# Kernel optimization log

Hardware: AMD Instinct MI355X
Metric: run time of the kernel (lower is better)

Reference implementation:

```python
import jax, jax.numpy as jnp
import numpy as np

NUM_HEADS = 4

def _ln(h, g, b, eps=1e-5):
    m = jnp.mean(h, axis=-1, keepdims=True)
    v = jnp.var(h, axis=-1, keepdims=True)
    return (h - m) / jnp.sqrt(v + eps) * g + b

def setup_inputs() -> dict:
    N, E, dn, de, da, H = 10000, 320000, 128, 128, 128, NUM_HEADS
    d_n, d_e, d_o = dn // H, de // H, da // H
    keys = iter(jax.random.split(jax.random.key(0), 64))
    def rn(shape, s=0.02):
        return jax.random.normal(next(keys), shape, dtype=jnp.float32) * s
    inp = {
        'x': jax.random.normal(next(keys), (N, dn), dtype=jnp.float32),
        'edge_feature': jax.random.normal(next(keys), (E, de), dtype=jnp.float32),
        'edge_index': jax.random.randint(next(keys), (2, E), 0, N, dtype=jnp.int32),
        # edge_gate: Linear(de, de//2) -> ReLU -> BN(eval, identity stats) -> Linear(de//2, 1) -> Sigmoid
        'Wg1': rn((de, de // 2)), 'bg1': jnp.zeros((de // 2,), jnp.float32),
        'Wg2': rn((de // 2, 1)), 'bg2': jnp.zeros((1,), jnp.float32),
        # nn_edge: build_mlp([2dn+2de, dn+2de, de]), Linear-ReLU-Linear
        'We1': rn((2 * dn + 2 * de, dn + 2 * de)), 'be1': jnp.zeros((dn + 2 * de,), jnp.float32),
        'We2': rn((dn + 2 * de, de)), 'be2': jnp.zeros((de,), jnp.float32),
        # edge LayerNorm
        'ge': jnp.ones((de,), jnp.float32), 'beta_e': jnp.zeros((de,), jnp.float32),
        # projections (single Linear each)
        'Wq': rn((dn, dn)), 'bq': jnp.zeros((dn,), jnp.float32),
        'Wpe': rn((de, de)), 'bpe': jnp.zeros((de,), jnp.float32),
        'Wv': rn((dn, da)), 'bv': jnp.zeros((da,), jnp.float32),
        # attention MLP (Conv1d kernel-1 over channel dim): [d_n+d_e, d_n+d_e, d_o]
        'A1': rn((d_n + d_e, d_n + d_e)), 'a1': jnp.zeros((d_n + d_e,), jnp.float32),
        'A2': rn((d_o, d_n + d_e)), 'a2': jnp.zeros((d_o,), jnp.float32),
        # twinning linear (shared; original re-inits per node, see notes): [2*de -> da]
        'Wt': rn((2 * de, da)), 'bt': jnp.zeros((da,), jnp.float32),
        # prop: build_mlp([dn+da, dn+da, dn])
        'Wp1': rn((dn + da, dn + da)), 'bp1': jnp.zeros((dn + da,), jnp.float32),
        'Wp2': rn((dn + da, dn)), 'bp2': jnp.zeros((dn,), jnp.float32),
        # final LayerNorm
        'gn': jnp.ones((dn,), jnp.float32), 'bn': jnp.zeros((dn,), jnp.float32),
    }
    return inp

def reference(x, edge_feature, edge_index, Wg1, bg1, Wg2, bg2, We1, be1, We2, be2,
              ge, beta_e, Wq, bq, Wpe, bpe, Wv, bv, A1, a1, A2, a2, Wt, bt,
              Wp1, bp1, Wp2, bp2, gn, bn):
    N, E = x.shape[0], edge_index.shape[1]
    H = NUM_HEADS
    src, dst = edge_index[0], edge_index[1]
    x_i = x[src]            # [E, dn]  (flow target_to_source: i = edge_index[0])
    x_j = x[dst]            # [E, dn]
    # --- reverse-edge lookup, vectorized via sorted key search ---
    key = src.astype(jnp.int64) * N + dst.astype(jnp.int64)
    rkey = dst.astype(jnp.int64) * N + src.astype(jnp.int64)
    order = jnp.argsort(key)
    sk = key[order]
    pos = jnp.clip(jnp.searchsorted(sk, rkey), 0, E - 1)
    found = sk[pos] == rkey
    rev_feat = jnp.where(found[:, None], edge_feature[order[pos]], 0.0)
    # --- edge gate (BatchNorm in eval with default stats == identity) ---
    g = jax.nn.relu(edge_feature @ Wg1 + bg1)
    gates = jax.nn.sigmoid(g @ Wg2 + bg2)   # [E,1]
    rev_feat = gates * rev_feat
    # --- MultiHeadedEdgeAttention ---
    ef = jnp.concatenate([x_i, edge_feature, rev_feat, x_j], axis=1)  # [E, 2dn+2de]
    ef = jax.nn.relu(ef @ We1 + be1) @ We2 + be2
    gcn_edge_feature = _ln(ef, ge, beta_e)                            # [E, de]
    value = x_j @ Wv + bv                                             # [E, da]
    q = (x_i @ Wq + bq).reshape(E, -1, H)                             # [E, d_n, H]
    e = (edge_feature @ Wpe + bpe).reshape(E, -1, H)                  # [E, d_e, H]
    h = jnp.concatenate([q, e], axis=1)                               # [E, d_n+d_e, H]
    h = jax.nn.relu(jnp.einsum('bch,oc->boh', h, A1) + a1[None, :, None])
    prob = jnp.einsum('bch,oc->boh', h, A2) + a2[None, :, None]       # [E, d_o, H]
    prob = jax.nn.softmax(prob, axis=1)
    xx_e = prob.reshape(E, -1) * value                                # [E, da]
    # --- scatter-max aggregate at src (dim_size N), empty segments -> 0 ---
    seg = jax.ops.segment_max(xx_e, src, num_segments=N)
    ones = jnp.ones((E,), jnp.float32)
    cnt_s = jax.ops.segment_sum(ones, src, num_segments=N)
    cnt_d = jax.ops.segment_sum(ones, dst, num_segments=N)
    xx = jnp.where(cnt_s[:, None] > 0, seg, 0.0)                      # [N, da]
    # --- twinning edge attention: mean of gcn edge features per subject/object ---
    subj = jax.ops.segment_sum(gcn_edge_feature, src, num_segments=N) / jnp.maximum(cnt_s, 1.0)[:, None]
    obj = jax.ops.segment_sum(gcn_edge_feature, dst, num_segments=N) / jnp.maximum(cnt_d, 1.0)[:, None]
    twin = jnp.concatenate([subj, obj], axis=1) @ Wt + bt             # [N, da]
    xx = jax.nn.relu(xx) * jax.nn.sigmoid(twin)
    xx = jnp.concatenate([x, xx], axis=1)
    xx = jax.nn.relu(xx @ Wp1 + bp1) @ Wp2 + bp2
    xx = _ln(xx, gn, bn)
    return (xx, gcn_edge_feature)
```

## Files before the change

### kernel.cpp

```cpp
#include <hip/hip_runtime.h>

#define N_NODES 10000
#define N_EDGES 320000
#define HASH_LOG 20
#define HASH_SZ (1 << HASH_LOG)
#define HASH_MASK (HASH_SZ - 1)
#define EMPTY_KEY 0xFFFFFFFFu

typedef unsigned int u32;
typedef unsigned short u16;
typedef __attribute__((ext_vector_type(8))) short bf16x8;
typedef __attribute__((ext_vector_type(4))) float f32x4;

__device__ __forceinline__ float bf2f(u16 v) {
    return __uint_as_float(((u32)v) << 16);
}
__device__ __forceinline__ u16 f2b(float f) {
    u32 x = __float_as_uint(f);
    return (u16)((x + 0x7FFFu + ((x >> 16) & 1u)) >> 16);
}
__device__ __forceinline__ void unpack8(uint4 u, float* f) {
    f[0] = __uint_as_float(u.x << 16); f[1] = __uint_as_float(u.x & 0xFFFF0000u);
    f[2] = __uint_as_float(u.y << 16); f[3] = __uint_as_float(u.y & 0xFFFF0000u);
    f[4] = __uint_as_float(u.z << 16); f[5] = __uint_as_float(u.z & 0xFFFF0000u);
    f[6] = __uint_as_float(u.w << 16); f[7] = __uint_as_float(u.w & 0xFFFF0000u);
}
__device__ __forceinline__ bf16x8 pack8(float4 a, float4 b) {
    union { bf16x8 v; u32 u[4]; } r;
    r.u[0] = (u32)f2b(a.x) | ((u32)f2b(a.y) << 16);
    r.u[1] = (u32)f2b(a.z) | ((u32)f2b(a.w) << 16);
    r.u[2] = (u32)f2b(b.x) | ((u32)f2b(b.y) << 16);
    r.u[3] = (u32)f2b(b.z) | ((u32)f2b(b.w) << 16);
    return r.v;
}

__global__ __launch_bounds__(256) void k_hash_build(
    const int* __restrict__ ei, u32* __restrict__ hkey, int* __restrict__ hval,
    int* __restrict__ cs, int* __restrict__ cd)
{
    int e = blockIdx.x * 256 + threadIdx.x;
    int s = ei[e], d = ei[N_EDGES + e];
    atomicAdd(&cs[s], 1);
    atomicAdd(&cd[d], 1);
    u32 key = (u32)(s * N_NODES + d);
    u32 h = (key * 2654435761u) >> (32 - HASH_LOG);
    for (;;) {
        u32 prev = atomicCAS(&hkey[h], EMPTY_KEY, key);
        if (prev == EMPTY_KEY || prev == key) { atomicMin(&hval[h], e); break; }
        h = (h + 1) & HASH_MASK;
    }
}

__global__ __launch_bounds__(256) void k_rev_lookup(
    const int* __restrict__ ei, const u32* __restrict__ hkey,
    const int* __restrict__ hval, int* __restrict__ rev)
{
    int e = blockIdx.x * 256 + threadIdx.x;
    int s = ei[e], d = ei[N_EDGES + e];
    u32 rkey = (u32)(d * N_NODES + s);
    u32 h = (rkey * 2654435761u) >> (32 - HASH_LOG);
    int r = -1;
    for (;;) {
        u32 k = hkey[h];
        if (k == EMPTY_KEY) break;
        if (k == rkey) { r = hval[h]; break; }
        h = (h + 1) & HASH_MASK;
    }
    rev[e] = r;
}

__global__ __launch_bounds__(256) void k_scan(
    const int* __restrict__ cs, const int* __restrict__ cd,
    int* __restrict__ off_s, int* __restrict__ off_d)
{
    __shared__ int sums[256];
    const int t = threadIdx.x;
    const int C = 40;
    const int* src = (blockIdx.x == 0) ? cs : cd;
    int* dst = (blockIdx.x == 0) ? off_s : off_d;
    int lo = t * C;
    int s = 0;
    for (int i = 0; i < C; i++) {
        int idx = lo + i;
        if (idx < N_NODES) s += src[idx];
    }
    sums[t] = s;
    __syncthreads();
    if (t == 0) {
        int acc = 0;
        for (int i = 0; i < 256; i++) { int v = sums[i]; sums[i] = acc; acc += v; }
    }
    __syncthreads();
    int acc = sums[t];
    for (int i = 0; i < C; i++) {
        int idx = lo + i;
        if (idx < N_NODES) { dst[idx] = acc; acc += src[idx]; }
    }
    if (t == 0) dst[N_NODES] = N_EDGES;
}

__global__ __launch_bounds__(256) void k_bucket(
    const int* __restrict__ ei, const int* __restrict__ off_s,
    const int* __restrict__ off_d, int* __restrict__ cur_s,
    int* __restrict__ cur_d, int* __restrict__ csr_es, int* __restrict__ csr_ed)
{
    int e = blockIdx.x * 256 + threadIdx.x;
    int s = ei[e], d = ei[N_EDGES + e];
    int ps = off_s[s] + atomicAdd(&cur_s[s], 1);
    csr_es[ps] = e;
    int pd = off_d[d] + atomicAdd(&cur_d[d], 1);
    csr_ed[pd] = e;
}

__global__ __launch_bounds__(256) void k_wconv(
    const float* __restrict__ src, u16* __restrict__ dst, int n)
{
    int i = blockIdx.x * 256 + threadIdx.x;
    if (i < n) dst[i] = f2b(src[i]);
}

__global__ __launch_bounds__(256) void k_wpackfrag(
    const float* __restrict__ src, u16* __restrict__ dst,
    int K, int Nn, int r0, int ld)
{
    int g = blockIdx.x * 256 + threadIdx.x;
    int ntc = Nn >> 4;
    int total = (K >> 5) * ntc * 64;
    if (g >= total) return;
    int lane = g & 63;
    int f = g >> 6;
    int nt = f % ntc, kc = f / ntc;
    int lq = lane & 15, q8 = lane >> 4;
    const float* s = src + (size_t)(r0 + kc * 32 + q8 * 8) * ld + nt * 16 + lq;
    u32 out[4];
#pragma unroll
    for (int j = 0; j < 4; j++) {
        float v0 = s[(size_t)(2 * j) * ld], v1 = s[(size_t)(2 * j + 1) * ld];
        out[j] = (u32)f2b(v0) | ((u32)f2b(v1) << 16);
    }
    *(uint4*)(dst + (size_t)g * 8) = make_uint4(out[0], out[1], out[2], out[3]);
}

__global__ __launch_bounds__(256) void k_node_proj(
    const float* __restrict__ x,
    const float* __restrict__ Wq, const float* __restrict__ bq,
    const float* __restrict__ Wv, const float* __restrict__ bv,
    const float* __restrict__ We1, const float* __restrict__ be1,
    u16* __restrict__ xq, u16* __restrict__ xv,
    u16* __restrict__ Pn, u16* __restrict__ Qn)
{
    __shared__ float XT[128 * 36];
    __shared__ float Ws[16 * 128];
    const int t = threadIdx.x;
    const int nb = blockIdx.x, y = blockIdx.y;
    const int n0 = nb * 32;
    {
        int nl = t & 31;
        int n = n0 + nl; if (n >= N_NODES) n = N_NODES - 1;
        int k0 = (t >> 5) * 16;
        const float4* xp = (const float4*)(x + (size_t)n * 128 + k0);
#pragma unroll
        for (int i = 0; i < 4; i++) {
            float4 v = xp[i];
            XT[(k0 + 4 * i + 0) * 36 + nl] = v.x;
            XT[(k0 + 4 * i + 1) * 36 + nl] = v.y;
            XT[(k0 + 4 * i + 2) * 36 + nl] = v.z;
            XT[(k0 + 4 * i + 3) * 36 + nl] = v.w;
        }
    }
    const int col = t & 127, rb = t >> 7;
    float acc[16];
#pragma unroll
    for (int j = 0; j < 16; j++) acc[j] = 0.f;
    for (int kc = 0; kc < 8; kc++) {
        __syncthreads();
#pragma unroll
        for (int i = 0; i < 2; i++) {
            int f4 = t + 256 * i;
            int row = f4 >> 5, c4 = (f4 & 31) * 4;
            int kg = kc * 16 + row;
            const float* srcw;
            if (y == 0)      srcw = Wq + (size_t)kg * 128 + c4;
            else if (y == 1) srcw = Wv + (size_t)kg * 128 + c4;
            else if (y < 5)  srcw = We1 + (size_t)kg * 384 + (y - 2) * 128 + c4;
            else             srcw = We1 + (size_t)(384 + kg) * 384 + (y - 5) * 128 + c4;
            *(float4*)&Ws[row * 128 + c4] = *(const float4*)srcw;
        }
        __syncthreads();
#pragma unroll
        for (int k = 0; k < 16; k++) {
            float w = Ws[k * 128 + col];
            const float4* ap = (const float4*)&XT[(kc * 16 + k) * 36 + rb * 16];
            float4 a0 = ap[0], a1v = ap[1], a2v = ap[2], a3v = ap[3];
            float ar[16] = {a0.x,a0.y,a0.z,a0.w, a1v.x,a1v.y,a1v.z,a1v.w,
                            a2v.x,a2v.y,a2v.z,a2v.w, a3v.x,a3v.y,a3v.z,a3v.w};
#pragma unroll
            for (int j = 0; j < 16; j++) acc[j] = fmaf(ar[j], w, acc[j]);
        }
    }
    float bias = 0.f;
    if (y == 0) bias = bq[col];
    else if (y == 1) bias = bv[col];
    else if (y < 5) bias = be1[(y - 2) * 128 + col];
#pragma unroll
    for (int j = 0; j < 16; j++) {
        int n = n0 + rb * 16 + j;
        if (n >= N_NODES) continue;
        u16 v = f2b(acc[j] + bias);
        if (y == 0)      xq[(size_t)n * 128 + col] = v;
        else if (y == 1) xv[(size_t)n * 128 + col] = v;
        else if (y < 5)  Pn[(size_t)n * 384 + (y - 2) * 128 + col] = v;
        else             Qn[(size_t)n * 384 + (y - 5) * 128 + col] = v;
    }
}

__global__ __launch_bounds__(256) void k_gates(
    const float* __restrict__ ef,
    const float* __restrict__ Wg1, const float* __restrict__ bg1,
    const float* __restrict__ Wg2, const float* __restrict__ bg2,
    float* __restrict__ gates)
{
    __shared__ float Wg1s[128 * 64];
    __shared__ float EFT[32 * 68];
    const int t = threadIdx.x;
    const int e0 = blockIdx.x * 64;
#pragma unroll
    for (int i = 0; i < 8; i++) {
        int f4 = t + 256 * i;
        *(float4*)&Wg1s[f4 * 4] = *(const float4*)&Wg1[f4 * 4];
    }
    const int o = t & 63, eb = t >> 6;
    float acc[16];
#pragma unroll
    for (int j = 0; j < 16; j++) acc[j] = 0.f;
    for (int kc = 0; kc < 4; kc++) {
        __syncthreads();
        {
            int e = t & 63, kk = (t >> 6) * 8;
            const float4* p = (const float4*)&ef[(size_t)(e0 + e) * 128 + kc * 32 + kk];
            float4 v0 = p[0], v1 = p[1];
            EFT[(kk + 0) * 68 + e] = v0.x; EFT[(kk + 1) * 68 + e] = v0.y;
            EFT[(kk + 2) * 68 + e] = v0.z; EFT[(kk + 3) * 68 + e] = v0.w;
            EFT[(kk + 4) * 68 + e] = v1.x; EFT[(kk + 5) * 68 + e] = v1.y;
            EFT[(kk + 6) * 68 + e] = v1.z; EFT[(kk + 7) * 68 + e] = v1.w;
        }
        __syncthreads();
#pragma unroll
        for (int k = 0; k < 32; k++) {
            const float4* ap = (const float4*)&EFT[k * 68 + eb * 16];
            float4 a0 = ap[0], a1v = ap[1], a2v = ap[2], a3v = ap[3];
            float w = Wg1s[(kc * 32 + k) * 64 + o];
            float ar[16] = {a0.x,a0.y,a0.z,a0.w, a1v.x,a1v.y,a1v.z,a1v.w,
                            a2v.x,a2v.y,a2v.z,a2v.w, a3v.x,a3v.y,a3v.z,a3v.w};
#pragma unroll
            for (int j = 0; j < 16; j++) acc[j] = fmaf(ar[j], w, acc[j]);
        }
    }
    float b1 = bg1[o], w2 = Wg2[o], b2 = bg2[0];
#pragma unroll
    for (int j = 0; j < 16; j++) {
        float v = fmaxf(acc[j] + b1, 0.f) * w2;
#pragma unroll
        for (int off = 32; off > 0; off >>= 1) v += __shfl_xor(v, off, 64);
        if ((t & 63) == 0)
            gates[e0 + eb * 16 + j] = 1.f / (1.f + __expf(-(v + b2)));
    }
}

__global__ __launch_bounds__(256, 3) void k_edge_mlp(
    const float* __restrict__ ef, const int* __restrict__ ei,
    const int* __restrict__ rev, const float* __restrict__ gates,
    const u16* __restrict__ Pn, const u16* __restrict__ Qn,
    const u16* __restrict__ We1p, const u16* __restrict__ We2p,
    const float* __restrict__ be2, const float* __restrict__ ge,
    const float* __restrict__ beta_e,
    float* __restrict__ out_gcn)
{
    __shared__ char ldsbuf[50176];
    __shared__ int srcs[64], dsts[64], revs[64];
    __shared__ float gts[64];
    u16* Abuf = (u16*)ldsbuf;
    u16* H1   = (u16*)ldsbuf;

    const int t = threadIdx.x;
    const int e0 = blockIdx.x * 64;
    const int w = t >> 6, lane = t & 63, q8 = lane >> 4, lq = lane & 15;

    if (t < 64) {
        srcs[t] = ei[e0 + t]; dsts[t] = ei[N_EDGES + e0 + t];
        revs[t] = rev[e0 + t]; gts[t] = gates[e0 + t];
    }
    __syncthreads();
    {
        int r = t >> 2, part = t & 3;
        int e = e0 + r;
        u16* arow = Abuf + r * 264;
        const float* efr = ef + (size_t)e * 128 + part * 32;
#pragma unroll
        for (int i = 0; i < 8; i++) {
            float4 v = *(const float4*)(efr + i * 4);
            u32 lo = (u32)f2b(v.x) | ((u32)f2b(v.y) << 16);
            u32 hi = (u32)f2b(v.z) | ((u32)f2b(v.w) << 16);
            *(uint2*)&arow[part * 32 + i * 4] = make_uint2(lo, hi);
        }
        int rv = revs[r];
        float g = gts[r];
        if (rv >= 0) {
            const float* rr = ef + (size_t)rv * 128 + part * 32;
#pragma unroll
            for (int i = 0; i < 8; i++) {
                float4 v = *(const float4*)(rr + i * 4);
                u32 lo = (u32)f2b(v.x * g) | ((u32)f2b(v.y * g) << 16);
                u32 hi = (u32)f2b(v.z * g) | ((u32)f2b(v.w * g) << 16);
                *(uint2*)&arow[128 + part * 32 + i * 4] = make_uint2(lo, hi);
            }
        } else {
#pragma unroll
            for (int i = 0; i < 8; i++)
                *(uint2*)&arow[128 + part * 32 + i * 4] = make_uint2(0u, 0u);
        }
    }
    __syncthreads();
    f32x4 acc1[4][6];
#pragma unroll
    for (int mt = 0; mt < 4; mt++)
#pragma unroll
        for (int nt = 0; nt < 6; nt++) acc1[mt][nt] = (f32x4){0.f, 0.f, 0.f, 0.f};
    {
        const u16* Bp = We1p + ((size_t)(w * 6) * 64 + lane) * 8;
#pragma unroll 2
        for (int kc = 0; kc < 8; kc++) {
            bf16x8 af[4], bfr[6];
#pragma unroll
            for (int mt = 0; mt < 4; mt++)
                af[mt] = *(const bf16x8*)(Abuf + (mt * 16 + lq) * 264 + kc * 32 + q8 * 8);
#pragma unroll
            for (int nt = 0; nt < 6; nt++)
                bfr[nt] = *(const bf16x8*)(Bp + (size_t)kc * 12288 + nt * 512);
#pragma unroll
            for (int mt = 0; mt < 4; mt++)
#pragma unroll
                for (int nt = 0; nt < 6; nt++)
                    acc1[mt][nt] = __builtin_amdgcn_mfma_f32_16x16x32_bf16(
                        af[mt], bfr[nt], acc1[mt][nt], 0, 0, 0);
        }
    }
    __syncthreads();
#pragma unroll
    for (int mt = 0; mt < 4; mt++) {
        int m = mt * 16 + q8 * 4;
#pragma unroll
        for (int nt = 0; nt < 6; nt++) {
            int c = w * 96 + nt * 16 + lq;
#pragma unroll
            for (int r = 0; r < 4; r++)
                H1[(m + r) * 392 + c] = f2b(acc1[mt][nt][r]);
        }
    }
    __syncthreads();
    {
        int r = t >> 2, cb = (t & 3) * 96;
        const u16* pr = Pn + (size_t)srcs[r] * 384;
        const u16* qr = Qn + (size_t)dsts[r] * 384;
        u16* hr = H1 + r * 392;
#pragma unroll
        for (int i = 0; i < 12; i++) {
            int c = cb + i * 8;
            uint4 hv = *(uint4*)&hr[c];
            uint4 pv = *(const uint4*)&pr[c];
            uint4 qv = *(const uint4*)&qr[c];
            float hf[8], pf[8], qf[8];
            unpack8(hv, hf); unpack8(pv, pf); unpack8(qv, qf);
            u16 o[8];
#pragma unroll
            for (int j = 0; j < 8; j++) o[j] = f2b(fmaxf(hf[j] + pf[j] + qf[j], 0.f));
            uint4 ov;
            ov.x = (u32)o[0] | ((u32)o[1] << 16);
            ov.y = (u32)o[2] | ((u32)o[3] << 16);
            ov.z = (u32)o[4] | ((u32)o[5] << 16);
            ov.w = (u32)o[6] | ((u32)o[7] << 16);
            *(uint4*)&hr[c] = ov;
        }
    }
    __syncthreads();
    f32x4 acc2[8];
#pragma unroll
    for (int nt = 0; nt < 8; nt++) acc2[nt] = (f32x4){0.f, 0.f, 0.f, 0.f};
    {
        const u16* Bp2 = We2p + (size_t)lane * 8;
#pragma unroll 2
        for (int kc = 0; kc < 12; kc++) {
            bf16x8 a = *(const bf16x8*)(H1 + (w * 16 + lq) * 392 + kc * 32 + q8 * 8);
#pragma unroll
            for (int nt = 0; nt < 8; nt++) {
                bf16x8 b = *(const bf16x8*)(Bp2 + (size_t)kc * 4096 + nt * 512);
                acc2[nt] = __builtin_amdgcn_mfma_f32_16x16x32_bf16(a, b, acc2[nt], 0, 0, 0);
            }
        }
    }
    {
        float be2v[8], gev[8], bev[8];
#pragma unroll
        for (int nt = 0; nt < 8; nt++) {
            int c = nt * 16 + lq;
            be2v[nt] = be2[c]; gev[nt] = ge[c]; bev[nt] = beta_e[c];
        }
#pragma unroll
        for (int r = 0; r < 4; r++) {
            int m = w * 16 + q8 * 4 + r;
            int e = e0 + m;
            float vals[8];
            float s = 0.f, sq = 0.f;
#pragma unroll
            for (int nt = 0; nt < 8; nt++) {
                float v = acc2[nt][r] + be2v[nt];
                vals[nt] = v; s += v; sq += v * v;
            }
#pragma unroll
            for (int off = 8; off > 0; off >>= 1) {
                s += __shfl_xor(s, off, 64);
                sq += __shfl_xor(sq, off, 64);
            }
            float mean = s * (1.f / 128.f);
            float var = sq * (1.f / 128.f) - mean * mean;
            float rstd = rsqrtf(var + 1e-5f);
            float* og = out_gcn + (size_t)e * 128;
#pragma unroll
            for (int nt = 0; nt < 8; nt++) {
                int c = nt * 16 + lq;
                og[c] = (vals[nt] - mean) * rstd * gev[nt] + bev[nt];
            }
        }
    }
}

__device__ __forceinline__ int hswz(int r, int c) {
    int g = ((c >> 3) ^ r ^ (r >> 3)) & 7;
    return r * 128 + (g << 4) + ((c & 7) << 1);
}

__global__ __launch_bounds__(256, 5) void k_atten(
    const float* __restrict__ ef, const int* __restrict__ ei,
    const u16* __restrict__ xq, const u16* __restrict__ xv,
    const u16* __restrict__ Wpep, const float* __restrict__ bpe,
    const u16* __restrict__ A1b, const float* __restrict__ a1,
    const u16* __restrict__ A2b, const float* __restrict__ a2,
    u16* __restrict__ xxe)
{
    __shared__ __align__(16) char lds[32768];
    const int t = threadIdx.x;
    const int e0 = blockIdx.x * 64;
    const int w = t >> 6, lane = t & 63, q8 = lane >> 4, lq = lane & 15;
    char* Hw = lds + w * 8192;
    const int ew0 = e0 + w * 16;

    {
        int el = lane >> 2, part = lane & 3;
        int sn = ei[ew0 + el];
        const uint4* p = (const uint4*)(xq + (size_t)sn * 128 + part * 32);
        int r0 = el * 4;
#pragma unroll
        for (int i = 0; i < 4; i++) {
            uint4 v = p[i];
            int c0 = part * 8 + i * 2;
            *(u32*)(Hw + hswz(r0 + 0, c0)) = (v.x & 0xFFFFu) | (v.z << 16);
            *(u32*)(Hw + hswz(r0 + 1, c0)) = (v.x >> 16) | (v.z & 0xFFFF0000u);
            *(u32*)(Hw + hswz(r0 + 2, c0)) = (v.y & 0xFFFFu) | (v.w << 16);
            *(u32*)(Hw + hswz(r0 + 3, c0)) = (v.y >> 16) | (v.w & 0xFFFF0000u);
        }
    }
    f32x4 acc1[8];
#pragma unroll
    for (int nt = 0; nt < 8; nt++) acc1[nt] = (f32x4){0.f, 0.f, 0.f, 0.f};
    {
        const u16* Bp = Wpep + (size_t)lane * 8;
#pragma unroll
        for (int kc = 0; kc < 4; kc++) {
            const float* ar = ef + (size_t)(ew0 + lq) * 128 + kc * 32 + q8 * 8;
            float4 v0 = ((const float4*)ar)[0];
            float4 v1 = ((const float4*)ar)[1];
            bf16x8 a = pack8(v0, v1);
#pragma unroll
            for (int nt = 0; nt < 8; nt++) {
                bf16x8 b = *(const bf16x8*)(Bp + (size_t)(kc * 8 + nt) * 512);
                acc1[nt] = __builtin_amdgcn_mfma_f32_16x16x32_bf16(
                    a, b, acc1[nt], 0, 0, 0);
            }
        }
    }
    {
#pragma unroll
        for (int nt = 0; nt < 8; nt++) {
            int j = nt * 16 + lq;
            int c = 32 + (j >> 2), hh = j & 3;
            float bb = bpe[j];
#pragma unroll
            for (int r = 0; r < 4; r++) {
                int el = q8 * 4 + r;
                *(u16*)(Hw + hswz(el * 4 + hh, c)) = f2b(acc1[nt][r] + bb);
            }
        }
    }
    f32x4 acc2[4][4];
#pragma unroll
    for (int mt = 0; mt < 4; mt++)
#pragma unroll
        for (int nt = 0; nt < 4; nt++) acc2[mt][nt] = (f32x4){0.f, 0.f, 0.f, 0.f};
#pragma unroll
    for (int kc = 0; kc < 2; kc++) {
        bf16x8 af[4], bfr[4];
#pragma unroll
        for (int mt = 0; mt < 4; mt++)
            af[mt] = *(const bf16x8*)(Hw + hswz(mt * 16 + lq, kc * 32 + q8 * 8));
#pragma unroll
        for (int nt = 0; nt < 4; nt++)
            bfr[nt] = *(const bf16x8*)(A1b + (size_t)(nt * 16 + lq) * 64 + kc * 32 + q8 * 8);
#pragma unroll
        for (int mt = 0; mt < 4; mt++)
#pragma unroll
            for (int nt = 0; nt < 4; nt++)
                acc2[mt][nt] = __builtin_amdgcn_mfma_f32_16x16x32_bf16(
                    af[mt], bfr[nt], acc2[mt][nt], 0, 0, 0);
    }
    {
        float a1v[4];
#pragma unroll
        for (int nt = 0; nt < 4; nt++) a1v[nt] = a1[nt * 16 + lq];
#pragma unroll
        for (int mt = 0; mt < 4; mt++)
#pragma unroll
            for (int nt = 0; nt < 4; nt++)
#pragma unroll
                for (int r = 0; r < 4; r++)
                    *(u16*)(Hw + hswz(mt * 16 + q8 * 4 + r, nt * 16 + lq)) =
                        f2b(fmaxf(acc2[mt][nt][r] + a1v[nt], 0.f));
    }
    f32x4 acc3[4][2];
#pragma unroll
    for (int mt = 0; mt < 4; mt++)
#pragma unroll
        for (int nt = 0; nt < 2; nt++) acc3[mt][nt] = (f32x4){0.f, 0.f, 0.f, 0.f};
#pragma unroll
    for (int kc = 0; kc < 2; kc++) {
        bf16x8 af[4], bfr[2];
#pragma unroll
        for (int mt = 0; mt < 4; mt++)
            af[mt] = *(const bf16x8*)(Hw + hswz(mt * 16 + lq, kc * 32 + q8 * 8));
#pragma unroll
        for (int nt = 0; nt < 2; nt++)
            bfr[nt] = *(const bf16x8*)(A2b + (size_t)(nt * 16 + lq) * 64 + kc * 32 + q8 * 8);
#pragma unroll
        for (int mt = 0; mt < 4; mt++)
#pragma unroll
            for (int nt = 0; nt < 2; nt++)
                acc3[mt][nt] = __builtin_amdgcn_mfma_f32_16x16x32_bf16(
                    af[mt], bfr[nt], acc3[mt][nt], 0, 0, 0);
    }
    {
        float a2v0 = a2[lq], a2v1 = a2[16 + lq];
#pragma unroll
        for (int mt = 0; mt < 4; mt++) {
#pragma unroll
            for (int r = 0; r < 4; r++) {
                float v0 = acc3[mt][0][r] + a2v0;
                float v1 = acc3[mt][1][r] + a2v1;
                float m = fmaxf(v0, v1);
#pragma unroll
                for (int off = 1; off < 16; off <<= 1)
                    m = fmaxf(m, __shfl_xor(m, off, 16));
                float p0 = __expf(v0 - m), p1 = __expf(v1 - m);
                float s = p0 + p1;
#pragma unroll
                for (int off = 1; off < 16; off <<= 1)
                    s += __shfl_xor(s, off, 16);
                float inv = 1.f / s;
                acc3[mt][0][r] = p0 * inv;
                acc3[mt][1][r] = p1 * inv;
            }
        }
    }
#pragma unroll
    for (int mt = 0; mt < 4; mt++) {
        int e = ew0 + mt * 4 + q8;
        int dn = ei[N_EDGES + e];
        const u16* vr = xv + (size_t)dn * 128;
        u16* xe = xxe + (size_t)e * 128;
#pragma unroll
        for (int nt = 0; nt < 2; nt++) {
            int o = nt * 16 + lq;
            uint2 vv = *(const uint2*)(vr + o * 4);
            float vf[4];
            vf[0] = bf2f((u16)(vv.x & 0xFFFFu)); vf[1] = bf2f((u16)(vv.x >> 16));
            vf[2] = bf2f((u16)(vv.y & 0xFFFFu)); vf[3] = bf2f((u16)(vv.y >> 16));
            u16 ov[4];
#pragma unroll
            for (int r = 0; r < 4; r++)
                ov[r] = f2b(fmaxf(acc3[mt][nt][r] * vf[r], 0.f));
            uint2 pk;
            pk.x = (u32)ov[0] | ((u32)ov[1] << 16);
            pk.y = (u32)ov[2] | ((u32)ov[3] << 16);
            *(uint2*)(xe + o * 4) = pk;
        }
    }
}

__global__ __launch_bounds__(256) void k_aggregate(
    const int* __restrict__ off_s, const int* __restrict__ off_d,
    const int* __restrict__ csr_es, const int* __restrict__ csr_ed,
    const u16* __restrict__ xxe, const float* __restrict__ gcn,
    float* __restrict__ xx, float* __restrict__ subj, float* __restrict__ obj)
{
    const int t = threadIdx.x;
    const int lane = t & 63, w = t >> 6;
    const int n = blockIdx.x * 4 + w;
    int s0 = off_s[n], s1 = off_s[n + 1];
    float mx0 = 0.f, mx1 = 0.f;
    float sb0 = 0.f, sb1 = 0.f;
    for (int i = s0; i < s1; i++) {
        int e = csr_es[i];
        u32 v = *(const u32*)(xxe + (size_t)e * 128 + 2 * lane);
        mx0 = fmaxf(mx0, bf2f((u16)(v & 0xFFFFu)));
        mx1 = fmaxf(mx1, bf2f((u16)(v >> 16)));
        float2 g = *(const float2*)&gcn[(size_t)e * 128 + 2 * lane];
        sb0 += g.x; sb1 += g.y;
    }
    int d0 = off_d[n], d1 = off_d[n + 1];
    float ob0 = 0.f, ob1 = 0.f;
    for (int i = d0; i < d1; i++) {
        int e = csr_ed[i];
        float2 g = *(const float2*)&gcn[(size_t)e * 128 + 2 * lane];
        ob0 += g.x; ob1 += g.y;
    }
    *(float2*)&xx[(size_t)n * 128 + 2 * lane] = make_float2(mx0, mx1);
    *(float2*)&subj[(size_t)n * 128 + 2 * lane] = make_float2(sb0, sb1);
    *(float2*)&obj[(size_t)n * 128 + 2 * lane] = make_float2(ob0, ob1);
}

__global__ __launch_bounds__(256) void k_node_final(
    const float* __restrict__ x, const float* __restrict__ subj,
    const float* __restrict__ obj, const int* __restrict__ cs,
    const int* __restrict__ cd, const float* __restrict__ xxbuf,
    const float* __restrict__ Wt, const float* __restrict__ bt,
    const float* __restrict__ Wp1, const float* __restrict__ bp1,
    const float* __restrict__ Wp2, const float* __restrict__ bp2,
    const float* __restrict__ gn, const float* __restrict__ bn,
    float* __restrict__ out)
{
    __shared__ float sc[4][4][256];
    const int t = threadIdx.x;
    const int lane = t & 63, w = t >> 6;
    const int n0 = blockIdx.x * 16 + w * 4;
#pragma unroll
    for (int nn = 0; nn < 4; nn++) {
        int n = n0 + nn;
        float inv_s = 1.f / fmaxf((float)cs[n], 1.f);
        float inv_d = 1.f / fmaxf((float)cd[n], 1.f);
#pragma unroll
        for (int i = 0; i < 4; i++) {
            int c = lane + 64 * i;
            float v = (c < 128) ? subj[(size_t)n * 128 + c] * inv_s
                                : obj[(size_t)n * 128 + (c - 128)] * inv_d;
            sc[w][nn][c] = v;
        }
    }
    __syncthreads();
    float a8[4][2];
#pragma unroll
    for (int nn = 0; nn < 4; nn++) { a8[nn][0] = 0.f; a8[nn][1] = 0.f; }
#pragma unroll 4
    for (int k = 0; k < 256; k++) {
        float2 wv = *(const float2*)&Wt[(size_t)k * 128 + 2 * lane];
#pragma unroll
        for (int nn = 0; nn < 4; nn++) {
            float h = sc[w][nn][k];
            a8[nn][0] = fmaf(h, wv.x, a8[nn][0]);
            a8[nn][1] = fmaf(h, wv.y, a8[nn][1]);
        }
    }
    __syncthreads();
    {
        float bt0 = bt[2 * lane], bt1 = bt[2 * lane + 1];
#pragma unroll
        for (int nn = 0; nn < 4; nn++) {
            int n = n0 + nn;
            float tw0 = a8[nn][0] + bt0, tw1 = a8[nn][1] + bt1;
            float xx0 = xxbuf[(size_t)n * 128 + 2 * lane] * (1.f / (1.f + __expf(-tw0)));
            float xx1 = xxbuf[(size_t)n * 128 + 2 * lane + 1] * (1.f / (1.f + __expf(-tw1)));
            float2 xv2 = *(const float2*)&x[(size_t)n * 128 + 2 * lane];
            sc[w][nn][2 * lane] = xv2.x;
            sc[w][nn][2 * lane + 1] = xv2.y;
            sc[w][nn][128 + 2 * lane] = xx0;
            sc[w][nn][129 + 2 * lane] = xx1;
        }
    }
    __syncthreads();
    float a16[4][4];
#pragma unroll
    for (int nn = 0; nn < 4; nn++)
#pragma unroll
        for (int j = 0; j < 4; j++) a16[nn][j] = 0.f;
#pragma unroll 4
    for (int k = 0; k < 256; k++) {
        float4 wv = *(const float4*)&Wp1[(size_t)k * 256 + 4 * lane];
#pragma unroll
        for (int nn = 0; nn < 4; nn++) {
            float h = sc[w][nn][k];
            a16[nn][0] = fmaf(h, wv.x, a16[nn][0]);
            a16[nn][1] = fmaf(h, wv.y, a16[nn][1]);
            a16[nn][2] = fmaf(h, wv.z, a16[nn][2]);
            a16[nn][3] = fmaf(h, wv.w, a16[nn][3]);
        }
    }
    __syncthreads();
    {
        float q0 = bp1[4 * lane], q1 = bp1[4 * lane + 1];
        float q2 = bp1[4 * lane + 2], q3 = bp1[4 * lane + 3];
#pragma unroll
        for (int nn = 0; nn < 4; nn++) {
            sc[w][nn][4 * lane + 0] = fmaxf(a16[nn][0] + q0, 0.f);
            sc[w][nn][4 * lane + 1] = fmaxf(a16[nn][1] + q1, 0.f);
            sc[w][nn][4 * lane + 2] = fmaxf(a16[nn][2] + q2, 0.f);
            sc[w][nn][4 * lane + 3] = fmaxf(a16[nn][3] + q3, 0.f);
        }
    }
    __syncthreads();
    float a8b[4][2];
#pragma unroll
    for (int nn = 0; nn < 4; nn++) { a8b[nn][0] = 0.f; a8b[nn][1] = 0.f; }
#pragma unroll 4
    for (int k = 0; k < 256; k++) {
        float2 wv = *(const float2*)&Wp2[(size_t)k * 128 + 2 * lane];
#pragma unroll
        for (int nn = 0; nn < 4; nn++) {
            float h = sc[w][nn][k];
            a8b[nn][0] = fmaf(h, wv.x, a8b[nn][0]);
            a8b[nn][1] = fmaf(h, wv.y, a8b[nn][1]);
        }
    }
    float bpa = bp2[2 * lane], bpb = bp2[2 * lane + 1];
    float g0 = gn[2 * lane], g1v = gn[2 * lane + 1];
    float b0 = bn[2 * lane], b1v = bn[2 * lane + 1];
#pragma unroll
    for (int nn = 0; nn < 4; nn++) {
        float v0 = a8b[nn][0] + bpa, v1 = a8b[nn][1] + bpb;
        float s = v0 + v1, sq = v0 * v0 + v1 * v1;
#pragma unroll
        for (int off = 32; off > 0; off >>= 1) {
            s += __shfl_xor(s, off, 64);
            sq += __shfl_xor(sq, off, 64);
        }
        float m = s * (1.f / 128.f);
        float var = sq * (1.f / 128.f) - m * m;
        float rstd = rsqrtf(var + 1e-5f);
        float2 o2;
        o2.x = (v0 - m) * rstd * g0 + b0;
        o2.y = (v1 - m) * rstd * g1v + b1v;
        *(float2*)&out[(size_t)(n0 + nn) * 128 + 2 * lane] = o2;
    }
}

extern "C" void kernel_launch(void* const* d_in, const int* in_sizes, int n_in,
                              void* d_out, int out_size, void* d_ws, size_t ws_size,
                              hipStream_t stream) {
    const float* x     = (const float*)d_in[0];
    const float* ef    = (const float*)d_in[1];
    const int*   ei    = (const int*)d_in[2];
    const float* Wg1   = (const float*)d_in[3];
    const float* bg1   = (const float*)d_in[4];
    const float* Wg2   = (const float*)d_in[5];
    const float* bg2   = (const float*)d_in[6];
    const float* We1   = (const float*)d_in[7];
    const float* be1   = (const float*)d_in[8];
    const float* We2   = (const float*)d_in[9];
    const float* be2   = (const float*)d_in[10];
    const float* ge    = (const float*)d_in[11];
    const float* betae = (const float*)d_in[12];
    const float* Wq    = (const float*)d_in[13];
    const float* bq    = (const float*)d_in[14];
    const float* Wpe   = (const float*)d_in[15];
    const float* bpe   = (const float*)d_in[16];
    const float* Wv    = (const float*)d_in[17];
    const float* bv    = (const float*)d_in[18];
    const float* A1    = (const float*)d_in[19];
    const float* a1    = (const float*)d_in[20];
    const float* A2    = (const float*)d_in[21];
    const float* a2    = (const float*)d_in[22];
    const float* Wt    = (const float*)d_in[23];
    const float* bt    = (const float*)d_in[24];
    const float* Wp1   = (const float*)d_in[25];
    const float* bp1   = (const float*)d_in[26];
    const float* Wp2   = (const float*)d_in[27];
    const float* bp2   = (const float*)d_in[28];
    const float* gn    = (const float*)d_in[29];
    const float* bn    = (const float*)d_in[30];

    char* ws = (char*)d_ws;
    size_t off = 0;
    auto take = [&](size_t b) -> void* {
        void* p = ws + off;
        off = (off + b + 255) & ~(size_t)255;
        return p;
    };
    u32*  hkey   = (u32*)take((size_t)HASH_SZ * 4);
    int*  hval   = (int*)take((size_t)HASH_SZ * 4);
    int*  rev    = (int*)take((size_t)N_EDGES * 4);
    float* gates = (float*)take((size_t)N_EDGES * 4);
    u16*  xq     = (u16*)take((size_t)N_NODES * 128 * 2);
    u16*  xv     = (u16*)take((size_t)N_NODES * 128 * 2);
    u16*  Pn     = (u16*)take((size_t)N_NODES * 384 * 2);
    u16*  Qn     = (u16*)take((size_t)N_NODES * 384 * 2);
    u16*  We1p   = (u16*)take((size_t)384 * 256 * 2);
    u16*  We2p   = (u16*)take((size_t)128 * 384 * 2);
    u16*  Wpep   = (u16*)take((size_t)128 * 128 * 2);
    u16*  A1b    = (u16*)take((size_t)64 * 64 * 2);
    u16*  A2b    = (u16*)take((size_t)32 * 64 * 2);
    u16*  xxe    = (u16*)take((size_t)N_EDGES * 128 * 2);
    float* xxbuf = (float*)take((size_t)N_NODES * 128 * 4);
    float* subj  = (float*)take((size_t)N_NODES * 128 * 4);
    float* obj   = (float*)take((size_t)N_NODES * 128 * 4);
    int*  off_s  = (int*)take((size_t)(N_NODES + 1) * 4);
    int*  off_d  = (int*)take((size_t)(N_NODES + 1) * 4);
    int*  csr_es = (int*)take((size_t)N_EDGES * 4);
    int*  csr_ed = (int*)take((size_t)N_EDGES * 4);
    int*  cs     = (int*)take((size_t)N_NODES * 4);
    int*  cd     = (int*)take((size_t)N_NODES * 4);
    int*  cur_s  = (int*)take((size_t)N_NODES * 4);
    int*  cur_d  = (int*)take((size_t)N_NODES * 4);
    size_t zbytes = (size_t)((ws + off) - (char*)cs);

    hipMemsetAsync(hkey, 0xFF, (size_t)HASH_SZ * 4, stream);
    hipMemsetAsync(hval, 0x7F, (size_t)HASH_SZ * 4, stream);
    hipMemsetAsync(cs, 0, zbytes, stream);

    float* out_xx  = (float*)d_out;
    float* out_gcn = (float*)d_out + (size_t)N_NODES * 128;

    k_hash_build<<<N_EDGES / 256, 256, 0, stream>>>(ei, hkey, hval, cs, cd);
    k_rev_lookup<<<N_EDGES / 256, 256, 0, stream>>>(ei, hkey, hval, rev);
    k_scan<<<2, 256, 0, stream>>>(cs, cd, off_s, off_d);
    k_bucket<<<N_EDGES / 256, 256, 0, stream>>>(
        ei, off_s, off_d, cur_s, cur_d, csr_es, csr_ed);
    k_wpackfrag<<<48, 256, 0, stream>>>(We1, We1p, 256, 384, 128, 384);
    k_wpackfrag<<<24, 256, 0, stream>>>(We2, We2p, 384, 128, 0, 128);
    k_wpackfrag<<<8, 256, 0, stream>>>(Wpe, Wpep, 128, 128, 0, 128);
    k_wconv<<<16, 256, 0, stream>>>(A1, A1b, 64 * 64);
    k_wconv<<<8, 256, 0, stream>>>(A2, A2b, 32 * 64);
    k_node_proj<<<dim3((N_NODES + 31) / 32, 8), 256, 0, stream>>>(
        x, Wq, bq, Wv, bv, We1, be1, xq, xv, Pn, Qn);
    k_gates<<<N_EDGES / 64, 256, 0, stream>>>(ef, Wg1, bg1, Wg2, bg2, gates);
    k_edge_mlp<<<N_EDGES / 64, 256, 0, stream>>>(
        ef, ei, rev, gates, Pn, Qn, We1p, We2p, be2, ge, betae, out_gcn);
    k_atten<<<N_EDGES / 64, 256, 0, stream>>>(
        ef, ei, xq, xv, Wpep, bpe, A1b, a1, A2b, a2, xxe);
    k_aggregate<<<N_NODES / 4, 256, 0, stream>>>(
        off_s, off_d, csr_es, csr_ed, xxe, out_gcn, xxbuf, subj, obj);
    k_node_final<<<N_NODES / 16, 256, 0, stream>>>(
        x, subj, obj, cs, cd, xxbuf, Wt, bt, Wp1, bp1, Wp2, bp2, gn, bn, out_xx);
}
```

Before: 1.240 ms.

## Pre-convert edge features to bf16 and widen edge MLP to 512 threads

Adds a one-off kernel that converts edge_feature to bf16 so the edge MLP and attention kernels read half the bytes and skip per-use conversion. The edge MLP kernel moves from 256 to 512 threads per block, splitting the N dimension of both GEMMs across 8 waves. This needs an LDS cross-wave reduction for the LayerNorm statistics. The cost is an extra pass over the 164 MB edge tensor, plus extra workspace and an extra barrier. The reverse-edge features are now rounded to bf16 before the gate multiply, so they are rounded twice.

```diff
diff --git a/kernel.cpp b/kernel.cpp
--- a/kernel.cpp
+++ b/kernel.cpp
@@ -110,6 +110,16 @@
     csr_es[ps] = e;
     int pd = off_d[d] + atomicAdd(&cur_d[d], 1);
     csr_ed[pd] = e;
+}
+
+__global__ __launch_bounds__(256) void k_conv8(
+    const float* __restrict__ src, u16* __restrict__ dst, int n8)
+{
+    int i = blockIdx.x * 256 + threadIdx.x;
+    if (i >= n8) return;
+    const float4* p = (const float4*)(src + (size_t)i * 8);
+    bf16x8 v = pack8(p[0], p[1]);
+    *(bf16x8*)(dst + (size_t)i * 8) = v;
 }
 
 __global__ __launch_bounds__(256) void k_wconv(
@@ -267,8 +277,8 @@
     }
 }
 
-__global__ __launch_bounds__(256, 3) void k_edge_mlp(
-    const float* __restrict__ ef, const int* __restrict__ ei,
+__global__ __launch_bounds__(512, 6) void k_edge_mlp(
+    const u16* __restrict__ efb, const int* __restrict__ ei,
     const int* __restrict__ rev, const float* __restrict__ gates,
     const u16* __restrict__ Pn, const u16* __restrict__ Qn,
     const u16* __restrict__ We1p, const u16* __restrict__ We2p,
@@ -277,6 +287,7 @@
     float* __restrict__ out_gcn)
 {
     __shared__ char ldsbuf[50176];
+    __shared__ float lnbuf[64][4];
     __shared__ int srcs[64], dsts[64], revs[64];
     __shared__ float gts[64];
     u16* Abuf = (u16*)ldsbuf;
@@ -292,55 +303,55 @@
     }
     __syncthreads();
     {
-        int r = t >> 2, part = t & 3;
-        int e = e0 + r;
+        int r = t >> 3, part = t & 7;
         u16* arow = Abuf + r * 264;
-        const float* efr = ef + (size_t)e * 128 + part * 32;
-#pragma unroll
-        for (int i = 0; i < 8; i++) {
-            float4 v = *(const float4*)(efr + i * 4);
-            u32 lo = (u32)f2b(v.x) | ((u32)f2b(v.y) << 16);
-            u32 hi = (u32)f2b(v.z) | ((u32)f2b(v.w) << 16);
-            *(uint2*)&arow[part * 32 + i * 4] = make_uint2(lo, hi);
-        }
+        const u16* er = efb + (size_t)(e0 + r) * 128 + part * 16;
+        *(uint4*)&arow[part * 16]     = *(const uint4*)er;
+        *(uint4*)&arow[part * 16 + 8] = *(const uint4*)(er + 8);
         int rv = revs[r];
         float g = gts[r];
         if (rv >= 0) {
-            const float* rr = ef + (size_t)rv * 128 + part * 32;
-#pragma unroll
-            for (int i = 0; i < 8; i++) {
-                float4 v = *(const float4*)(rr + i * 4);
-                u32 lo = (u32)f2b(v.x * g) | ((u32)f2b(v.y * g) << 16);
-                u32 hi = (u32)f2b(v.z * g) | ((u32)f2b(v.w * g) << 16);
-                *(uint2*)&arow[128 + part * 32 + i * 4] = make_uint2(lo, hi);
+            const u16* rr = efb + (size_t)rv * 128 + part * 16;
+#pragma unroll
+            for (int i = 0; i < 2; i++) {
+                uint4 v = ((const uint4*)rr)[i];
+                float f[8]; unpack8(v, f);
+                u16 o[8];
+#pragma unroll
+                for (int j = 0; j < 8; j++) o[j] = f2b(f[j] * g);
+                uint4 ov;
+                ov.x = (u32)o[0] | ((u32)o[1] << 16);
+                ov.y = (u32)o[2] | ((u32)o[3] << 16);
+                ov.z = (u32)o[4] | ((u32)o[5] << 16);
+                ov.w = (u32)o[6] | ((u32)o[7] << 16);
+                *(uint4*)&arow[128 + part * 16 + i * 8] = ov;
             }
         } else {
-#pragma unroll
-            for (int i = 0; i < 8; i++)
-                *(uint2*)&arow[128 + part * 32 + i * 4] = make_uint2(0u, 0u);
-        }
-    }
-    __syncthreads();
-    f32x4 acc1[4][6];
+            *(uint4*)&arow[128 + part * 16]     = make_uint4(0u, 0u, 0u, 0u);
+            *(uint4*)&arow[128 + part * 16 + 8] = make_uint4(0u, 0u, 0u, 0u);
+        }
+    }
+    __syncthreads();
+    f32x4 acc1[4][3];
 #pragma unroll
     for (int mt = 0; mt < 4; mt++)
 #pragma unroll
-        for (int nt = 0; nt < 6; nt++) acc1[mt][nt] = (f32x4){0.f, 0.f, 0.f, 0.f};
-    {
-        const u16* Bp = We1p + ((size_t)(w * 6) * 64 + lane) * 8;
+        for (int nt = 0; nt < 3; nt++) acc1[mt][nt] = (f32x4){0.f, 0.f, 0.f, 0.f};
+    {
+        const u16* Bp = We1p + ((size_t)(w * 3) * 64 + lane) * 8;
 #pragma unroll 2
         for (int kc = 0; kc < 8; kc++) {
-            bf16x8 af[4], bfr[6];
+            bf16x8 af[4], bfr[3];
 #pragma unroll
             for (int mt = 0; mt < 4; mt++)
                 af[mt] = *(const bf16x8*)(Abuf + (mt * 16 + lq) * 264 + kc * 32 + q8 * 8);
 #pragma unroll
-            for (int nt = 0; nt < 6; nt++)
+            for (int nt = 0; nt < 3; nt++)
                 bfr[nt] = *(const bf16x8*)(Bp + (size_t)kc * 12288 + nt * 512);
 #pragma unroll
             for (int mt = 0; mt < 4; mt++)
 #pragma unroll
-                for (int nt = 0; nt < 6; nt++)
+                for (int nt = 0; nt < 3; nt++)
                     acc1[mt][nt] = __builtin_amdgcn_mfma_f32_16x16x32_bf16(
                         af[mt], bfr[nt], acc1[mt][nt], 0, 0, 0);
         }
@@ -350,8 +361,8 @@
     for (int mt = 0; mt < 4; mt++) {
         int m = mt * 16 + q8 * 4;
 #pragma unroll
-        for (int nt = 0; nt < 6; nt++) {
-            int c = w * 96 + nt * 16 + lq;
+        for (int nt = 0; nt < 3; nt++) {
+            int c = w * 48 + nt * 16 + lq;
 #pragma unroll
             for (int r = 0; r < 4; r++)
                 H1[(m + r) * 392 + c] = f2b(acc1[mt][nt][r]);
@@ -359,12 +370,12 @@
     }
     __syncthreads();
     {
-        int r = t >> 2, cb = (t & 3) * 96;
+        int r = t >> 3, cb = (t & 7) * 48;
         const u16* pr = Pn + (size_t)srcs[r] * 384;
         const u16* qr = Qn + (size_t)dsts[r] * 384;
         u16* hr = H1 + r * 392;
 #pragma unroll
-        for (int i = 0; i < 12; i++) {
+        for (int i = 0; i < 6; i++) {
             int c = cb + i * 8;
             uint4 hv = *(uint4*)&hr[c];
             uint4 pv = *(const uint4*)&pr[c];
@@ -383,53 +394,62 @@
         }
     }
     __syncthreads();
-    f32x4 acc2[8];
-#pragma unroll
-    for (int nt = 0; nt < 8; nt++) acc2[nt] = (f32x4){0.f, 0.f, 0.f, 0.f};
-    {
-        const u16* Bp2 = We2p + (size_t)lane * 8;
+    const int rb2 = (w & 3) * 16, ch = (w >> 2) * 64;
+    f32x4 acc2[4];
+#pragma unroll
+    for (int nt = 0; nt < 4; nt++) acc2[nt] = (f32x4){0.f, 0.f, 0.f, 0.f};
+    {
+        const u16* Bp2 = We2p + ((size_t)(w >> 2) * 4 * 64 + lane) * 8;
 #pragma unroll 2
         for (int kc = 0; kc < 12; kc++) {
-            bf16x8 a = *(const bf16x8*)(H1 + (w * 16 + lq) * 392 + kc * 32 + q8 * 8);
-#pragma unroll
-            for (int nt = 0; nt < 8; nt++) {
+            bf16x8 a = *(const bf16x8*)(H1 + (rb2 + lq) * 392 + kc * 32 + q8 * 8);
+#pragma unroll
+            for (int nt = 0; nt < 4; nt++) {
                 bf16x8 b = *(const bf16x8*)(Bp2 + (size_t)kc * 4096 + nt * 512);
                 acc2[nt] = __builtin_amdgcn_mfma_f32_16x16x32_bf16(a, b, acc2[nt], 0, 0, 0);
             }
         }
     }
-    {
-        float be2v[8], gev[8], bev[8];
-#pragma unroll
-        for (int nt = 0; nt < 8; nt++) {
-            int c = nt * 16 + lq;
-            be2v[nt] = be2[c]; gev[nt] = ge[c]; bev[nt] = beta_e[c];
-        }
-#pragma unroll
-        for (int r = 0; r < 4; r++) {
-            int m = w * 16 + q8 * 4 + r;
-            int e = e0 + m;
-            float vals[8];
-            float s = 0.f, sq = 0.f;
-#pragma unroll
-            for (int nt = 0; nt < 8; nt++) {
-                float v = acc2[nt][r] + be2v[nt];
-                vals[nt] = v; s += v; sq += v * v;
-            }
-#pragma unroll
-            for (int off = 8; off > 0; off >>= 1) {
-                s += __shfl_xor(s, off, 64);
-                sq += __shfl_xor(sq, off, 64);
-            }
-            float mean = s * (1.f / 128.f);
-            float var = sq * (1.f / 128.f) - mean * mean;
-            float rstd = rsqrtf(var + 1e-5f);
-            float* og = out_gcn + (size_t)e * 128;
-#pragma unroll
-            for (int nt = 0; nt < 8; nt++) {
-                int c = nt * 16 + lq;
-                og[c] = (vals[nt] - mean) * rstd * gev[nt] + bev[nt];
-            }
+    float be2v[4], gev[4], bev[4];
+#pragma unroll
+    for (int nt = 0; nt < 4; nt++) {
+        int c = ch + nt * 16 + lq;
+        be2v[nt] = be2[c]; gev[nt] = ge[c]; bev[nt] = beta_e[c];
+    }
+#pragma unroll
+    for (int r = 0; r < 4; r++) {
+        int m = rb2 + q8 * 4 + r;
+        float s = 0.f, sq = 0.f;
+#pragma unroll
+        for (int nt = 0; nt < 4; nt++) {
+            float v = acc2[nt][r] + be2v[nt];
+            s += v; sq += v * v;
+        }
+#pragma unroll
+        for (int off = 8; off > 0; off >>= 1) {
+            s += __shfl_xor(s, off, 64);
+            sq += __shfl_xor(sq, off, 64);
+        }
+        if (lq == 0) {
+            lnbuf[m][(w >> 2) * 2]     = s;
+            lnbuf[m][(w >> 2) * 2 + 1] = sq;
+        }
+    }
+    __syncthreads();
+#pragma unroll
+    for (int r = 0; r < 4; r++) {
+        int m = rb2 + q8 * 4 + r;
+        float s = lnbuf[m][0] + lnbuf[m][2];
+        float sq = lnbuf[m][1] + lnbuf[m][3];
+        float mean = s * (1.f / 128.f);
+        float var = sq * (1.f / 128.f) - mean * mean;
+        float rstd = rsqrtf(var + 1e-5f);
+        float* og = out_gcn + (size_t)(e0 + m) * 128;
+#pragma unroll
+        for (int nt = 0; nt < 4; nt++) {
+            int c = ch + nt * 16 + lq;
+            float v = acc2[nt][r] + be2v[nt];
+            og[c] = (v - mean) * rstd * gev[nt] + bev[nt];
         }
     }
 }
@@ -440,7 +460,7 @@
 }
 
 __global__ __launch_bounds__(256, 5) void k_atten(
-    const float* __restrict__ ef, const int* __restrict__ ei,
+    const u16* __restrict__ efb, const int* __restrict__ ei,
     const u16* __restrict__ xq, const u16* __restrict__ xv,
     const u16* __restrict__ Wpep, const float* __restrict__ bpe,
     const u16* __restrict__ A1b, const float* __restrict__ a1,
@@ -476,10 +496,7 @@
         const u16* Bp = Wpep + (size_t)lane * 8;
 #pragma unroll
         for (int kc = 0; kc < 4; kc++) {
-            const float* ar = ef + (size_t)(ew0 + lq) * 128 + kc * 32 + q8 * 8;
-            float4 v0 = ((const float4*)ar)[0];
-            float4 v1 = ((const float4*)ar)[1];
-            bf16x8 a = pack8(v0, v1);
+            bf16x8 a = *(const bf16x8*)(efb + (size_t)(ew0 + lq) * 128 + kc * 32 + q8 * 8);
 #pragma unroll
             for (int nt = 0; nt < 8; nt++) {
                 bf16x8 b = *(const bf16x8*)(Bp + (size_t)(kc * 8 + nt) * 512);
@@ -805,6 +822,7 @@
     int*  hval   = (int*)take((size_t)HASH_SZ * 4);
     int*  rev    = (int*)take((size_t)N_EDGES * 4);
     float* gates = (float*)take((size_t)N_EDGES * 4);
+    u16*  efb    = (u16*)take((size_t)N_EDGES * 128 * 2);
     u16*  xq     = (u16*)take((size_t)N_NODES * 128 * 2);
     u16*  xv     = (u16*)take((size_t)N_NODES * 128 * 2);
     u16*  Pn     = (u16*)take((size_t)N_NODES * 384 * 2);
@@ -837,6 +855,8 @@
 
     k_hash_build<<<N_EDGES / 256, 256, 0, stream>>>(ei, hkey, hval, cs, cd);
     k_rev_lookup<<<N_EDGES / 256, 256, 0, stream>>>(ei, hkey, hval, rev);
+    k_conv8<<<(N_EDGES * 128 / 8 + 255) / 256, 256, 0, stream>>>(
+        ef, efb, N_EDGES * 128 / 8);
     k_scan<<<2, 256, 0, stream>>>(cs, cd, off_s, off_d);
     k_bucket<<<N_EDGES / 256, 256, 0, stream>>>(
         ei, off_s, off_d, cur_s, cur_d, csr_es, csr_ed);
@@ -848,10 +868,10 @@
     k_node_proj<<<dim3((N_NODES + 31) / 32, 8), 256, 0, stream>>>(
         x, Wq, bq, Wv, bv, We1, be1, xq, xv, Pn, Qn);
     k_gates<<<N_EDGES / 64, 256, 0, stream>>>(ef, Wg1, bg1, Wg2, bg2, gates);
-    k_edge_mlp<<<N_EDGES / 64, 256, 0, stream>>>(
-        ef, ei, rev, gates, Pn, Qn, We1p, We2p, be2, ge, betae, out_gcn);
+    k_edge_mlp<<<N_EDGES / 64, 512, 0, stream>>>(
+        efb, ei, rev, gates, Pn, Qn, We1p, We2p, be2, ge, betae, out_gcn);
     k_atten<<<N_EDGES / 64, 256, 0, stream>>>(
-        ef, ei, xq, xv, Wpep, bpe, A1b, a1, A2b, a2, xxe);
+        efb, ei, xq, xv, Wpep, bpe, A1b, a1, A2b, a2, xxe);
     k_aggregate<<<N_NODES / 4, 256, 0, stream>>>(
         off_s, off_d, csr_es, csr_ed, xxe, out_gcn, xxbuf, subj, obj);
     k_node_final<<<N_NODES / 16, 256, 0, stream>>>(
```

After: 1.251 ms. About the same (+0.8%).
